# Performance work log

Hardware: AMD Instinct MI355X
Metric: run time of the kernel (lower is better)

## Reference

```python
import jax, jax.numpy as jnp
import numpy as np


def setup_inputs() -> dict:
    key = jax.random.key(0)
    k1, k2 = jax.random.split(key)
    q_embed = jax.random.normal(k1, (1000, 1024), dtype=jnp.float32)      # (V, D)
    conv_feat = jax.random.normal(k2, (64, 1024, 800), dtype=jnp.float32)  # (B, D, T)
    return {"q_embed": q_embed, "conv_feat": conv_feat}


def reference(q_embed, conv_feat):
    # sim_scores: (B, V, T) = q_embed (V, D) @ conv_feat (B, D, T), no scaling
    sim_scores = jnp.einsum('vd,bdt->bvt', q_embed, conv_feat)
    attention_weights = jax.nn.softmax(sim_scores, axis=2)  # over T
    # context: (B, V, D) = weights (B, V, T) @ conv_feat^T (B, T, D)
    context_vector = jnp.einsum('bvt,bdt->bvd', attention_weights, conv_feat)
    return (context_vector, attention_weights)
```

## Files before the change

kernel.cpp:

```cpp
#include <hip/hip_runtime.h>
#include <hip/hip_bf16.h>

typedef short bf16x8 __attribute__((ext_vector_type(8)));
typedef float f32x4 __attribute__((ext_vector_type(4)));

#define NV 1000
#define ND 1024
#define NT 800
#define NB 64

__device__ inline unsigned short f32_bf16(float f) {
    unsigned u = __builtin_bit_cast(unsigned, f);
    return (unsigned short)((u + 0x7FFFu + ((u >> 16) & 1u)) >> 16);
}
__device__ inline void split_bf16(float f, unsigned short& h, unsigned short& l) {
    unsigned u = __builtin_bit_cast(unsigned, f);
    unsigned hb = (u + 0x7FFFu + ((u >> 16) & 1u)) >> 16;
    h = (unsigned short)hb;
    float hf = __builtin_bit_cast(float, hb << 16);
    float lf = f - hf;
    unsigned ul = __builtin_bit_cast(unsigned, lf);
    l = (unsigned short)((ul + 0x7FFFu + ((ul >> 16) & 1u)) >> 16);
}

__device__ inline void gload16(const void* g, void* l) {
    __builtin_amdgcn_global_load_lds(
        (const __attribute__((address_space(1))) unsigned int*)g,
        (__attribute__((address_space(3))) unsigned int*)l, 16, 0, 0);
}

__global__ __launch_bounds__(256) void prep_q(const float* __restrict__ Q,
                                              unsigned short* __restrict__ Qh,
                                              unsigned short* __restrict__ Ql) {
    int idx = blockIdx.x * 256 + threadIdx.x;
    int row = idx >> 8;
    int c4 = (idx & 255) << 2;
    float4 f = make_float4(0.f, 0.f, 0.f, 0.f);
    if (row < NV) f = *(const float4*)(Q + (size_t)row * ND + c4);
    unsigned short h0,h1,h2,h3,l0,l1,l2,l3;
    split_bf16(f.x,h0,l0); split_bf16(f.y,h1,l1);
    split_bf16(f.z,h2,l2); split_bf16(f.w,h3,l3);
    *(ushort4*)(Qh + (size_t)row * ND + c4) = make_ushort4(h0,h1,h2,h3);
    *(ushort4*)(Ql + (size_t)row * ND + c4) = make_ushort4(l0,l1,l2,l3);
}

__global__ __launch_bounds__(256) void prep_c(const float* __restrict__ C,
                                              unsigned short* __restrict__ Cth,
                                              unsigned short* __restrict__ Ctl,
                                              unsigned short* __restrict__ Cbf,
                                              int writeCbf) {
    const int dt = blockIdx.x;
    const int tt = blockIdx.y;
    const int b  = blockIdx.z;
    const int tid = threadIdx.x;
    __shared__ float T[64][33];
    const float* Cb = C + (size_t)b * ND * NT;
    const int d0 = dt * 64, t0 = tt * 32;
#pragma unroll
    for (int r = 0; r < 2; ++r) {
        int idx = r * 256 + tid;
        int row = idx >> 3;
        int c4 = (idx & 7) << 2;
        float4 f = *(const float4*)(Cb + (size_t)(d0 + row) * NT + t0 + c4);
        T[row][c4 + 0] = f.x; T[row][c4 + 1] = f.y;
        T[row][c4 + 2] = f.z; T[row][c4 + 3] = f.w;
        if (writeCbf) {
            *(ushort4*)(Cbf + ((size_t)b * ND + d0 + row) * NT + t0 + c4) =
                make_ushort4(f32_bf16(f.x), f32_bf16(f.y), f32_bf16(f.z), f32_bf16(f.w));
        }
    }
    __syncthreads();
#pragma unroll
    for (int r = 0; r < 2; ++r) {
        int idx = r * 256 + tid;
        int trow = idx >> 4;
        int dc = (idx & 15) << 2;
        unsigned short h[4], l[4];
#pragma unroll
        for (int j = 0; j < 4; ++j) split_bf16(T[dc + j][trow], h[j], l[j]);
        size_t o = ((size_t)b * NT + t0 + trow) * ND + d0 + dc;
        *(ushort4*)(Cth + o) = make_ushort4(h[0],h[1],h[2],h[3]);
        *(ushort4*)(Ctl + o) = make_ushort4(l[0],l[1],l[2],l[3]);
    }
}

__global__ __launch_bounds__(256) void gemm1_kernel(const unsigned short* __restrict__ Qh,
                                                    const unsigned short* __restrict__ Ql,
                                                    const unsigned short* __restrict__ Cth,
                                                    const unsigned short* __restrict__ Ctl,
                                                    float* __restrict__ S) {
    const int h = blockIdx.x;
    const int L = (h & 7) * 320 + (h >> 3);
    const int bm = L & 7;
    const int rest = L >> 3;
    const int bn = rest % 5;
    const int b  = rest / 5;

    const int tid = threadIdx.x;
    const int lane = tid & 63;
    const int w = tid >> 6;
    const int wr = w >> 1, wc = w & 1;

    __shared__ unsigned short Ah[128 * 32];
    __shared__ unsigned short Al[128 * 32];
    __shared__ unsigned short Bh[160 * 32];
    __shared__ unsigned short Bl[160 * 32];

    const int v0 = bm * 128, t0 = bn * 160;
    const unsigned short* Agh = Qh + (size_t)v0 * ND;
    const unsigned short* Agl = Ql + (size_t)v0 * ND;
    const unsigned short* Bgh = Cth + ((size_t)b * NT + t0) * ND;
    const unsigned short* Bgl = Ctl + ((size_t)b * NT + t0) * ND;

    f32x4 acc[4][5];
#pragma unroll
    for (int i = 0; i < 4; ++i)
#pragma unroll
        for (int j = 0; j < 5; ++j) acc[i][j] = (f32x4){0.f, 0.f, 0.f, 0.f};

    const int srow = lane >> 2;
    const int sslot = lane & 3;
    const int swz = (sslot ^ (srow & 3) ^ ((srow >> 2) & 3)) << 3;

    for (int k0 = 0; k0 < ND; k0 += 32) {
        for (int i = w; i < 8; i += 4) {
            int row = i * 16 + srow;
            gload16(Agh + (size_t)row * ND + swz + k0, Ah + i * 512);
            gload16(Agl + (size_t)row * ND + swz + k0, Al + i * 512);
        }
        for (int i = w; i < 10; i += 4) {
            int row = i * 16 + srow;
            gload16(Bgh + (size_t)row * ND + swz + k0, Bh + i * 512);
            gload16(Bgl + (size_t)row * ND + swz + k0, Bl + i * 512);
        }
        __syncthreads();

        const int g = lane >> 4, rl = lane & 15;
        const int sx = (g ^ (rl & 3) ^ ((rl >> 2) & 3)) << 4;
        bf16x8 ah[4], al[4], bh[5], bl[5];
#pragma unroll
        for (int mf = 0; mf < 4; ++mf) {
            int off = (wr * 64 + mf * 16 + rl) * 64 + sx;
            ah[mf] = *(const bf16x8*)((const char*)Ah + off);
            al[mf] = *(const bf16x8*)((const char*)Al + off);
        }
#pragma unroll
        for (int nf = 0; nf < 5; ++nf) {
            int off = (wc * 80 + nf * 16 + rl) * 64 + sx;
            bh[nf] = *(const bf16x8*)((const char*)Bh + off);
            bl[nf] = *(const bf16x8*)((const char*)Bl + off);
        }
#pragma unroll
        for (int mf = 0; mf < 4; ++mf)
#pragma unroll
            for (int nf = 0; nf < 5; ++nf) {
                acc[mf][nf] = __builtin_amdgcn_mfma_f32_16x16x32_bf16(ah[mf], bh[nf], acc[mf][nf], 0, 0, 0);
                acc[mf][nf] = __builtin_amdgcn_mfma_f32_16x16x32_bf16(ah[mf], bl[nf], acc[mf][nf], 0, 0, 0);
                acc[mf][nf] = __builtin_amdgcn_mfma_f32_16x16x32_bf16(al[mf], bh[nf], acc[mf][nf], 0, 0, 0);
            }
        __syncthreads();
    }

    float* Sb = S + (size_t)b * NV * NT;
    const int g = lane >> 4, rl = lane & 15;
#pragma unroll
    for (int mf = 0; mf < 4; ++mf) {
#pragma unroll
        for (int nf = 0; nf < 5; ++nf) {
#pragma unroll
            for (int r = 0; r < 4; ++r) {
                int v = v0 + wr * 64 + mf * 16 + g * 4 + r;
                int t = t0 + wc * 80 + nf * 16 + rl;
                if (v < NV) Sb[(size_t)v * NT + t] = acc[mf][nf][r];
            }
        }
    }
}

__global__ __launch_bounds__(256) void softmax_kernel(float* __restrict__ S,
                                                      unsigned short* __restrict__ Wbf,
                                                      int writeWbf) {
    const int row = blockIdx.x * 4 + (threadIdx.x >> 6);
    const int lane = threadIdx.x & 63;
    float* p = S + (size_t)row * NT;
    unsigned short* pw = Wbf + (size_t)row * NT;
    float v[13];
    float m = -INFINITY;
#pragma unroll
    for (int i = 0; i < 13; ++i) {
        int t = i * 64 + lane;
        v[i] = (t < NT) ? p[t] : -INFINITY;
        m = fmaxf(m, v[i]);
    }
#pragma unroll
    for (int off = 32; off; off >>= 1) m = fmaxf(m, __shfl_xor(m, off));
    float s = 0.f;
#pragma unroll
    for (int i = 0; i < 13; ++i) {
        int t = i * 64 + lane;
        float e = (t < NT) ? __expf(v[i] - m) : 0.f;
        v[i] = e;
        s += e;
    }
#pragma unroll
    for (int off = 32; off; off >>= 1) s += __shfl_xor(s, off);
    const float inv = 1.0f / s;
#pragma unroll
    for (int i = 0; i < 13; ++i) {
        int t = i * 64 + lane;
        if (t < NT) {
            float wv = v[i] * inv;
            p[t] = wv;
            if (writeWbf) pw[t] = f32_bf16(wv);
        }
    }
}

__global__ __launch_bounds__(256) void gemm2_fast(const unsigned short* __restrict__ Wbf,
                                                  const unsigned short* __restrict__ Cbf,
                                                  float* __restrict__ O) {
    const int h = blockIdx.x;
    const int L = (h & 7) * 256 + (h >> 3);
    const int bm = L & 7;
    const int bn = (L >> 3) & 3;
    const int b  = L >> 5;
    const int tid = threadIdx.x;
    const int lane = tid & 63;
    const int w = tid >> 6;
    const int wr = w >> 1, wc = w & 1;

    __shared__ unsigned short As[128 * 32];
    __shared__ unsigned short Bs[256 * 32];

    const int v0 = bm * 128, d0 = bn * 256;
    const unsigned short* Ag = Wbf + (size_t)b * NV * NT;
    const unsigned short* Bg = Cbf + ((size_t)b * ND + d0) * NT;

    f32x4 acc[4][8];
#pragma unroll
    for (int i = 0; i < 4; ++i)
#pragma unroll
        for (int j = 0; j < 8; ++j) acc[i][j] = (f32x4){0.f, 0.f, 0.f, 0.f};

    const int srow = lane >> 2;
    const int sslot = lane & 3;
    const int swz = (sslot ^ (srow & 3) ^ ((srow >> 2) & 3)) << 3;

    for (int k0 = 0; k0 < NT; k0 += 32) {
        for (int i = w; i < 8; i += 4) {
            int row = i * 16 + srow;
            int vrow = v0 + row; if (vrow > NV - 1) vrow = NV - 1;
            gload16(Ag + (size_t)vrow * NT + swz + k0, As + i * 512);
        }
        for (int i = w; i < 16; i += 4) {
            int row = i * 16 + srow;
            gload16(Bg + (size_t)row * NT + swz + k0, Bs + i * 512);
        }
        __syncthreads();

        const int g = lane >> 4, rl = lane & 15;
        const int sx = (g ^ (rl & 3) ^ ((rl >> 2) & 3)) << 4;
        bf16x8 a[4], bfr[8];
#pragma unroll
        for (int mf = 0; mf < 4; ++mf) {
            int off = (wr * 64 + mf * 16 + rl) * 64 + sx;
            a[mf] = *(const bf16x8*)((const char*)As + off);
        }
#pragma unroll
        for (int nf = 0; nf < 8; ++nf) {
            int off = (wc * 128 + nf * 16 + rl) * 64 + sx;
            bfr[nf] = *(const bf16x8*)((const char*)Bs + off);
        }
#pragma unroll
        for (int mf = 0; mf < 4; ++mf)
#pragma unroll
            for (int nf = 0; nf < 8; ++nf)
                acc[mf][nf] = __builtin_amdgcn_mfma_f32_16x16x32_bf16(a[mf], bfr[nf], acc[mf][nf], 0, 0, 0);
        __syncthreads();
    }

    float* Ob = O + (size_t)b * NV * ND;
    const int g = lane >> 4, rl = lane & 15;
#pragma unroll
    for (int mf = 0; mf < 4; ++mf) {
#pragma unroll
        for (int nf = 0; nf < 8; ++nf) {
#pragma unroll
            for (int r = 0; r < 4; ++r) {
                int v = v0 + wr * 64 + mf * 16 + g * 4 + r;
                int d = d0 + wc * 128 + nf * 16 + rl;
                if (v < NV) Ob[(size_t)v * ND + d] = acc[mf][nf][r];
            }
        }
    }
}

__global__ __launch_bounds__(256) void gemm2_mid(const unsigned short* __restrict__ Wbf,
                                                 const float* __restrict__ C,
                                                 float* __restrict__ O) {
    const int h = blockIdx.x;
    const int L = (h & 7) * 512 + (h >> 3);
    const int bm = L & 7;
    const int bn = (L >> 3) & 7;
    const int b  = L >> 6;
    const int tid = threadIdx.x;
    const int lane = tid & 63;
    const int w = tid >> 6;
    const int wr = w >> 1, wc = w & 1;

    __shared__ unsigned short As[128 * 32];
    __shared__ unsigned short Bs[128][40];

    const int v0 = bm * 128, d0 = bn * 128;
    const unsigned short* Ag = Wbf + (size_t)b * NV * NT;
    const float* Cb = C + (size_t)b * ND * NT;

    f32x4 acc[4][4];
#pragma unroll
    for (int i = 0; i < 4; ++i)
#pragma unroll
        for (int j = 0; j < 4; ++j) acc[i][j] = (f32x4){0.f, 0.f, 0.f, 0.f};

    const int srow = lane >> 2;
    const int sslot = lane & 3;

    for (int k0 = 0; k0 < NT; k0 += 32) {
        for (int i = w; i < 8; i += 4) {
            int row = i * 16 + srow;
            int c = ((sslot ^ (row & 3)) << 3) + k0;
            int vrow = v0 + row; if (vrow > NV - 1) vrow = NV - 1;
            gload16(Ag + (size_t)vrow * NT + c, As + i * 512);
        }
#pragma unroll
        for (int r = 0; r < 4; ++r) {
            int idx = r * 256 + tid;
            int row = idx >> 3;
            int kq  = (idx & 7) << 2;
            const float4 f = *(const float4*)(Cb + (size_t)(d0 + row) * NT + k0 + kq);
            *(ushort4*)&Bs[row][kq] = make_ushort4(f32_bf16(f.x), f32_bf16(f.y), f32_bf16(f.z), f32_bf16(f.w));
        }
        __syncthreads();

        const int g = lane >> 4, rl = lane & 15;
        const int sx = (g ^ (rl & 3)) << 4;
        const int kk = g << 3;
        bf16x8 a[4], bfr[4];
#pragma unroll
        for (int mf = 0; mf < 4; ++mf) {
            int off = (wr * 64 + mf * 16 + rl) * 64 + sx;
            a[mf] = *(const bf16x8*)((const char*)As + off);
        }
#pragma unroll
        for (int nf = 0; nf < 4; ++nf) {
            int row = wc * 64 + nf * 16 + rl;
            bfr[nf] = *(const bf16x8*)&Bs[row][kk];
        }
#pragma unroll
        for (int mf = 0; mf < 4; ++mf)
#pragma unroll
            for (int nf = 0; nf < 4; ++nf)
                acc[mf][nf] = __builtin_amdgcn_mfma_f32_16x16x32_bf16(a[mf], bfr[nf], acc[mf][nf], 0, 0, 0);
        __syncthreads();
    }

    float* Ob = O + (size_t)b * NV * ND;
    const int g = lane >> 4, rl = lane & 15;
#pragma unroll
    for (int mf = 0; mf < 4; ++mf) {
#pragma unroll
        for (int nf = 0; nf < 4; ++nf) {
#pragma unroll
            for (int r = 0; r < 4; ++r) {
                int v = v0 + wr * 64 + mf * 16 + g * 4 + r;
                int d = d0 + wc * 64 + nf * 16 + rl;
                if (v < NV) Ob[(size_t)v * ND + d] = acc[mf][nf][r];
            }
        }
    }
}

__global__ __launch_bounds__(256) void gemm2_slow(const float* __restrict__ W,
                                                  const float* __restrict__ C,
                                                  float* __restrict__ O) {
    const int h = blockIdx.x;
    const int L = (h & 7) * 512 + (h >> 3);
    const int bm = L & 7;
    const int bn = (L >> 3) & 7;
    const int b  = L >> 6;
    const int tid = threadIdx.x;
    const int lane = tid & 63;
    const int wid = tid >> 6;
    const int wr = wid >> 1;
    const int wc = wid & 1;

    __shared__ unsigned short As[128][40];
    __shared__ unsigned short Bs[128][40];

    const float* Wb = W + (size_t)b * NV * NT;
    const float* Cb = C + (size_t)b * ND * NT;
    const int v0 = bm * 128;
    const int d0 = bn * 128;

    f32x4 acc[4][4];
#pragma unroll
    for (int i = 0; i < 4; ++i)
#pragma unroll
        for (int j = 0; j < 4; ++j) acc[i][j] = (f32x4){0.f, 0.f, 0.f, 0.f};

    for (int k0 = 0; k0 < NT; k0 += 32) {
#pragma unroll
        for (int r = 0; r < 4; ++r) {
            int idx = r * 256 + tid;
            int row = idx >> 3;
            int kq  = (idx & 7) << 2;
            int v = v0 + row; if (v > NV - 1) v = NV - 1;
            const float4 f = *(const float4*)(Wb + (size_t)v * NT + k0 + kq);
            *(ushort4*)&As[row][kq] = make_ushort4(f32_bf16(f.x), f32_bf16(f.y), f32_bf16(f.z), f32_bf16(f.w));
        }
#pragma unroll
        for (int r = 0; r < 4; ++r) {
            int idx = r * 256 + tid;
            int row = idx >> 3;
            int kq  = (idx & 7) << 2;
            const float4 f = *(const float4*)(Cb + (size_t)(d0 + row) * NT + k0 + kq);
            *(ushort4*)&Bs[row][kq] = make_ushort4(f32_bf16(f.x), f32_bf16(f.y), f32_bf16(f.z), f32_bf16(f.w));
        }
        __syncthreads();

        bf16x8 a[4], bfr[4];
        const int kk = (lane >> 4) << 3;
#pragma unroll
        for (int mf = 0; mf < 4; ++mf) {
            int row = wr * 64 + mf * 16 + (lane & 15);
            a[mf] = *(const bf16x8*)&As[row][kk];
        }
#pragma unroll
        for (int nf = 0; nf < 4; ++nf) {
            int row = wc * 64 + nf * 16 + (lane & 15);
            bfr[nf] = *(const bf16x8*)&Bs[row][kk];
        }
#pragma unroll
        for (int mf = 0; mf < 4; ++mf)
#pragma unroll
            for (int nf = 0; nf < 4; ++nf)
                acc[mf][nf] = __builtin_amdgcn_mfma_f32_16x16x32_bf16(a[mf], bfr[nf], acc[mf][nf], 0, 0, 0);
        __syncthreads();
    }

    float* Ob = O + (size_t)b * NV * ND;
#pragma unroll
    for (int mf = 0; mf < 4; ++mf) {
#pragma unroll
        for (int nf = 0; nf < 4; ++nf) {
#pragma unroll
            for (int r = 0; r < 4; ++r) {
                int v = v0 + wr * 64 + mf * 16 + (lane >> 4) * 4 + r;
                int d = d0 + wc * 64 + nf * 16 + (lane & 15);
                if (v < NV) Ob[(size_t)v * ND + d] = acc[mf][nf][r];
            }
        }
    }
}

extern "C" void kernel_launch(void* const* d_in, const int* in_sizes, int n_in,
                              void* d_out, int out_size, void* d_ws, size_t ws_size,
                              hipStream_t stream) {
    const float* Q = (const float*)d_in[0];
    const float* C = (const float*)d_in[1];
    float* ctx = (float*)d_out;
    float* wts = ctx + (size_t)NB * NV * ND;

    unsigned short* Cth = (unsigned short*)ctx;
    unsigned short* Ctl = Cth + (size_t)NB * NT * ND;
    unsigned short* Qh  = Ctl + (size_t)NB * NT * ND;
    unsigned short* Ql  = Qh + (size_t)1024 * ND;

    const size_t WbfBytes = (size_t)NB * NV * NT * 2;
    const size_t CbfBytes = (size_t)NB * ND * NT * 2;
    unsigned short* Wbf = (unsigned short*)d_ws;
    unsigned short* Cbf = (unsigned short*)((char*)d_ws + WbfBytes);
    const int wsFast = ws_size >= WbfBytes + CbfBytes;
    const int wsMid  = ws_size >= WbfBytes;

    prep_q<<<dim3(1024), 256, 0, stream>>>(Q, Qh, Ql);
    prep_c<<<dim3(16, 25, NB), 256, 0, stream>>>(C, Cth, Ctl, Cbf, wsFast);
    gemm1_kernel<<<dim3(2560), 256, 0, stream>>>(Qh, Ql, Cth, Ctl, wts);
    softmax_kernel<<<dim3(16000), 256, 0, stream>>>(wts, Wbf, wsMid);
    if (wsFast)      gemm2_fast<<<dim3(2048), 256, 0, stream>>>(Wbf, Cbf, ctx);
    else if (wsMid)  gemm2_mid<<<dim3(4096), 256, 0, stream>>>(Wbf, C, ctx);
    else             gemm2_slow<<<dim3(4096), 256, 0, stream>>>(wts, C, ctx);
}
```

Baseline: 728.1 us.

## Double-buffer LDS in both GEMMs and enlarge gemm2 tile to 256x256 with 512 threads

```diff
diff --git a/kernel.cpp b/kernel.cpp
--- a/kernel.cpp
+++ b/kernel.cpp
@@ -101,10 +101,7 @@
     const int w = tid >> 6;
     const int wr = w >> 1, wc = w & 1;
 
-    __shared__ unsigned short Ah[128 * 32];
-    __shared__ unsigned short Al[128 * 32];
-    __shared__ unsigned short Bh[160 * 32];
-    __shared__ unsigned short Bl[160 * 32];
+    __shared__ unsigned short lds[2][18432];
 
     const int v0 = bm * 128, t0 = bn * 160;
     const unsigned short* Agh = Qh + (size_t)v0 * ND;
@@ -121,48 +118,62 @@
     const int srow = lane >> 2;
     const int sslot = lane & 3;
     const int swz = (sslot ^ (srow & 3) ^ ((srow >> 2) & 3)) << 3;
-
-    for (int k0 = 0; k0 < ND; k0 += 32) {
-        for (int i = w; i < 8; i += 4) {
-            int row = i * 16 + srow;
-            gload16(Agh + (size_t)row * ND + swz + k0, Ah + i * 512);
-            gload16(Agl + (size_t)row * ND + swz + k0, Al + i * 512);
-        }
-        for (int i = w; i < 10; i += 4) {
-            int row = i * 16 + srow;
-            gload16(Bgh + (size_t)row * ND + swz + k0, Bh + i * 512);
-            gload16(Bgl + (size_t)row * ND + swz + k0, Bl + i * 512);
-        }
+    const int g = lane >> 4, rl = lane & 15;
+    const int sx = (g ^ (rl & 3) ^ ((rl >> 2) & 3)) << 4;
+
+#define G1_STAGE(K0, BUF)                                                     \
+    {                                                                         \
+        unsigned short* Lb = lds[BUF];                                        \
+        for (int i = w; i < 8; i += 4) {                                      \
+            int row = i * 16 + srow;                                          \
+            gload16(Agh + (size_t)row * ND + swz + (K0), Lb + i * 512);       \
+            gload16(Agl + (size_t)row * ND + swz + (K0), Lb + 4096 + i * 512);\
+        }                                                                     \
+        for (int i = w; i < 10; i += 4) {                                     \
+            int row = i * 16 + srow;                                          \
+            gload16(Bgh + (size_t)row * ND + swz + (K0), Lb + 8192 + i * 512);\
+            gload16(Bgl + (size_t)row * ND + swz + (K0), Lb + 13312 + i * 512);\
+        }                                                                     \
+    }
+
+#define G1_COMPUTE(BUF)                                                       \
+    {                                                                         \
+        const char* Lb = (const char*)lds[BUF];                               \
+        bf16x8 ah[4], al[4], bh[5], bl[5];                                    \
+        _Pragma("unroll")                                                     \
+        for (int mf = 0; mf < 4; ++mf) {                                      \
+            int off = (wr * 64 + mf * 16 + rl) * 64 + sx;                     \
+            ah[mf] = *(const bf16x8*)(Lb + off);                              \
+            al[mf] = *(const bf16x8*)(Lb + 8192 + off);                       \
+        }                                                                     \
+        _Pragma("unroll")                                                     \
+        for (int nf = 0; nf < 5; ++nf) {                                      \
+            int off = (wc * 80 + nf * 16 + rl) * 64 + sx;                     \
+            bh[nf] = *(const bf16x8*)(Lb + 16384 + off);                      \
+            bl[nf] = *(const bf16x8*)(Lb + 26624 + off);                      \
+        }                                                                     \
+        _Pragma("unroll")                                                     \
+        for (int mf = 0; mf < 4; ++mf)                                        \
+            _Pragma("unroll")                                                 \
+            for (int nf = 0; nf < 5; ++nf) {                                  \
+                acc[mf][nf] = __builtin_amdgcn_mfma_f32_16x16x32_bf16(ah[mf], bh[nf], acc[mf][nf], 0, 0, 0); \
+                acc[mf][nf] = __builtin_amdgcn_mfma_f32_16x16x32_bf16(ah[mf], bl[nf], acc[mf][nf], 0, 0, 0); \
+                acc[mf][nf] = __builtin_amdgcn_mfma_f32_16x16x32_bf16(al[mf], bh[nf], acc[mf][nf], 0, 0, 0); \
+            }                                                                 \
+    }
+
+    G1_STAGE(0, 0);
+    __syncthreads();
+    int cur = 0;
+    for (int t = 0; t < 31; ++t) {
+        G1_STAGE((t + 1) * 32, cur ^ 1);
+        G1_COMPUTE(cur);
         __syncthreads();
-
-        const int g = lane >> 4, rl = lane & 15;
-        const int sx = (g ^ (rl & 3) ^ ((rl >> 2) & 3)) << 4;
-        bf16x8 ah[4], al[4], bh[5], bl[5];
-#pragma unroll
-        for (int mf = 0; mf < 4; ++mf) {
-            int off = (wr * 64 + mf * 16 + rl) * 64 + sx;
-            ah[mf] = *(const bf16x8*)((const char*)Ah + off);
-            al[mf] = *(const bf16x8*)((const char*)Al + off);
-        }
-#pragma unroll
-        for (int nf = 0; nf < 5; ++nf) {
-            int off = (wc * 80 + nf * 16 + rl) * 64 + sx;
-            bh[nf] = *(const bf16x8*)((const char*)Bh + off);
-            bl[nf] = *(const bf16x8*)((const char*)Bl + off);
-        }
-#pragma unroll
-        for (int mf = 0; mf < 4; ++mf)
-#pragma unroll
-            for (int nf = 0; nf < 5; ++nf) {
-                acc[mf][nf] = __builtin_amdgcn_mfma_f32_16x16x32_bf16(ah[mf], bh[nf], acc[mf][nf], 0, 0, 0);
-                acc[mf][nf] = __builtin_amdgcn_mfma_f32_16x16x32_bf16(ah[mf], bl[nf], acc[mf][nf], 0, 0, 0);
-                acc[mf][nf] = __builtin_amdgcn_mfma_f32_16x16x32_bf16(al[mf], bh[nf], acc[mf][nf], 0, 0, 0);
-            }
-        __syncthreads();
-    }
+        cur ^= 1;
+    }
+    G1_COMPUTE(cur);
 
     float* Sb = S + (size_t)b * NV * NT;
-    const int g = lane >> 4, rl = lane & 15;
 #pragma unroll
     for (int mf = 0; mf < 4; ++mf) {
 #pragma unroll
@@ -175,6 +186,8 @@
             }
         }
     }
+#undef G1_STAGE
+#undef G1_COMPUTE
 }
 
 __global__ __launch_bounds__(256) void softmax_kernel(float* __restrict__ S,
@@ -216,83 +229,95 @@
     }
 }
 
-__global__ __launch_bounds__(256) void gemm2_fast(const unsigned short* __restrict__ Wbf,
+__global__ __launch_bounds__(512) void gemm2_fast(const unsigned short* __restrict__ Wbf,
                                                   const unsigned short* __restrict__ Cbf,
                                                   float* __restrict__ O) {
     const int h = blockIdx.x;
-    const int L = (h & 7) * 256 + (h >> 3);
-    const int bm = L & 7;
-    const int bn = (L >> 3) & 3;
-    const int b  = L >> 5;
+    const int L = (h & 7) * 128 + (h >> 3);
+    const int b  = L >> 4;
+    const int bm = (L >> 2) & 3;
+    const int bn = L & 3;
     const int tid = threadIdx.x;
     const int lane = tid & 63;
     const int w = tid >> 6;
-    const int wr = w >> 1, wc = w & 1;
-
-    __shared__ unsigned short As[128 * 32];
-    __shared__ unsigned short Bs[256 * 32];
-
-    const int v0 = bm * 128, d0 = bn * 256;
+    const int wr = w >> 2, wc = w & 3;
+
+    __shared__ unsigned short lds[2][16384];
+
+    const int v0 = bm * 256, d0 = bn * 256;
     const unsigned short* Ag = Wbf + (size_t)b * NV * NT;
     const unsigned short* Bg = Cbf + ((size_t)b * ND + d0) * NT;
 
-    f32x4 acc[4][8];
-#pragma unroll
-    for (int i = 0; i < 4; ++i)
-#pragma unroll
-        for (int j = 0; j < 8; ++j) acc[i][j] = (f32x4){0.f, 0.f, 0.f, 0.f};
+    f32x4 acc[8][4];
+#pragma unroll
+    for (int i = 0; i < 8; ++i)
+#pragma unroll
+        for (int j = 0; j < 4; ++j) acc[i][j] = (f32x4){0.f, 0.f, 0.f, 0.f};
 
     const int srow = lane >> 2;
     const int sslot = lane & 3;
     const int swz = (sslot ^ (srow & 3) ^ ((srow >> 2) & 3)) << 3;
-
-    for (int k0 = 0; k0 < NT; k0 += 32) {
-        for (int i = w; i < 8; i += 4) {
-            int row = i * 16 + srow;
-            int vrow = v0 + row; if (vrow > NV - 1) vrow = NV - 1;
-            gload16(Ag + (size_t)vrow * NT + swz + k0, As + i * 512);
-        }
-        for (int i = w; i < 16; i += 4) {
-            int row = i * 16 + srow;
-            gload16(Bg + (size_t)row * NT + swz + k0, Bs + i * 512);
-        }
+    const int g = lane >> 4, rl = lane & 15;
+    const int sx = (g ^ (rl & 3) ^ ((rl >> 2) & 3)) << 4;
+
+#define G2_STAGE(K0, BUF)                                                     \
+    {                                                                         \
+        unsigned short* Lb = lds[BUF];                                        \
+        for (int i = w; i < 16; i += 8) {                                     \
+            int row = i * 16 + srow;                                          \
+            int vrow = v0 + row; if (vrow > NV - 1) vrow = NV - 1;            \
+            gload16(Ag + (size_t)vrow * NT + swz + (K0), Lb + i * 512);       \
+            gload16(Bg + (size_t)row * NT + swz + (K0), Lb + 8192 + i * 512); \
+        }                                                                     \
+    }
+
+#define G2_COMPUTE(BUF)                                                       \
+    {                                                                         \
+        const char* Lb = (const char*)lds[BUF];                               \
+        bf16x8 a[8], bq[4];                                                   \
+        _Pragma("unroll")                                                     \
+        for (int mf = 0; mf < 8; ++mf) {                                      \
+            int off = (wr * 128 + mf * 16 + rl) * 64 + sx;                    \
+            a[mf] = *(const bf16x8*)(Lb + off);                               \
+        }                                                                     \
+        _Pragma("unroll")                                                     \
+        for (int nf = 0; nf < 4; ++nf) {                                      \
+            int off = (wc * 64 + nf * 16 + rl) * 64 + sx;                     \
+            bq[nf] = *(const bf16x8*)(Lb + 16384 + off);                      \
+        }                                                                     \
+        _Pragma("unroll")                                                     \
+        for (int mf = 0; mf < 8; ++mf)                                        \
+            _Pragma("unroll")                                                 \
+            for (int nf = 0; nf < 4; ++nf)                                    \
+                acc[mf][nf] = __builtin_amdgcn_mfma_f32_16x16x32_bf16(a[mf], bq[nf], acc[mf][nf], 0, 0, 0); \
+    }
+
+    G2_STAGE(0, 0);
+    __syncthreads();
+    int cur = 0;
+    for (int t = 0; t < 24; ++t) {
+        G2_STAGE((t + 1) * 32, cur ^ 1);
+        G2_COMPUTE(cur);
         __syncthreads();
-
-        const int g = lane >> 4, rl = lane & 15;
-        const int sx = (g ^ (rl & 3) ^ ((rl >> 2) & 3)) << 4;
-        bf16x8 a[4], bfr[8];
-#pragma unroll
-        for (int mf = 0; mf < 4; ++mf) {
-            int off = (wr * 64 + mf * 16 + rl) * 64 + sx;
-            a[mf] = *(const bf16x8*)((const char*)As + off);
-        }
-#pragma unroll
-        for (int nf = 0; nf < 8; ++nf) {
-            int off = (wc * 128 + nf * 16 + rl) * 64 + sx;
-            bfr[nf] = *(const bf16x8*)((const char*)Bs + off);
-        }
-#pragma unroll
-        for (int mf = 0; mf < 4; ++mf)
-#pragma unroll
-            for (int nf = 0; nf < 8; ++nf)
-                acc[mf][nf] = __builtin_amdgcn_mfma_f32_16x16x32_bf16(a[mf], bfr[nf], acc[mf][nf], 0, 0, 0);
-        __syncthreads();
-    }
+        cur ^= 1;
+    }
+    G2_COMPUTE(cur);
 
     float* Ob = O + (size_t)b * NV * ND;
-    const int g = lane >> 4, rl = lane & 15;
-#pragma unroll
-    for (int mf = 0; mf < 4; ++mf) {
-#pragma unroll
-        for (int nf = 0; nf < 8; ++nf) {
+#pragma unroll
+    for (int mf = 0; mf < 8; ++mf) {
+#pragma unroll
+        for (int nf = 0; nf < 4; ++nf) {
 #pragma unroll
             for (int r = 0; r < 4; ++r) {
-                int v = v0 + wr * 64 + mf * 16 + g * 4 + r;
-                int d = d0 + wc * 128 + nf * 16 + rl;
+                int v = v0 + wr * 128 + mf * 16 + g * 4 + r;
+                int d = d0 + wc * 64 + nf * 16 + rl;
                 if (v < NV) Ob[(size_t)v * ND + d] = acc[mf][nf][r];
             }
         }
     }
+#undef G2_STAGE
+#undef G2_COMPUTE
 }
 
 __global__ __launch_bounds__(256) void gemm2_mid(const unsigned short* __restrict__ Wbf,
@@ -486,7 +511,7 @@
     prep_c<<<dim3(16, 25, NB), 256, 0, stream>>>(C, Cth, Ctl, Cbf, wsFast);
     gemm1_kernel<<<dim3(2560), 256, 0, stream>>>(Qh, Ql, Cth, Ctl, wts);
     softmax_kernel<<<dim3(16000), 256, 0, stream>>>(wts, Wbf, wsMid);
-    if (wsFast)      gemm2_fast<<<dim3(2048), 256, 0, stream>>>(Wbf, Cbf, ctx);
+    if (wsFast)      gemm2_fast<<<dim3(1024), 512, 0, stream>>>(Wbf, Cbf, ctx);
     else if (wsMid)  gemm2_mid<<<dim3(4096), 256, 0, stream>>>(Wbf, C, ctx);
     else             gemm2_slow<<<dim3(4096), 256, 0, stream>>>(wts, C, ctx);
 }
```

New measurement: 705.7 us. -3.1%, faster.
